# Performance work log

Measured on AMD Instinct MI355X. Metric: run time of the kernel, lower is better.

## Reference

```python
import jax, jax.numpy as jnp
import numpy as np
from jax import lax

B_, DIM, H, W, Dd = 2, 256, 16, 16, 16
DI, N, DTR, K = 256, 8, 16, 4   # d_inner (expand=1), d_state, dt_rank=ceil(256/16), d_conv
OUT_C = 1200
L = H * W * Dd
EPS = 1e-5


def setup_inputs() -> dict:
    key = jax.random.key(0)
    ks = jax.random.split(key, 20)
    g = lambda k, s: jax.random.normal(k, s, jnp.float32) * 0.02
    A_log = jnp.log(jnp.broadcast_to(jnp.arange(1, N + 1, dtype=jnp.float32), (DI, N)))
    dt_bias = jnp.full((DI,), float(np.log(np.expm1(0.01))), jnp.float32)
    return {
        "input0": jax.random.normal(ks[0], (B_, DIM, H, W, Dd), jnp.float32),
        "input1": jax.random.normal(ks[1], (B_, DIM, H, W, Dd), jnp.float32),
        "norm0_w": jnp.ones((DIM,), jnp.float32),
        "norm0_b": jnp.zeros((DIM,), jnp.float32),
        "norm1_w": jnp.ones((DIM,), jnp.float32),
        "norm1_b": jnp.zeros((DIM,), jnp.float32),
        "in_proj_w": g(ks[2], (DI, DIM)),
        "in_projz_w": g(ks[3], (DI, DIM)),
        "conv1d_w": g(ks[4], (DI, 1, K)),
        "conv1d_bias": jnp.zeros((DI,), jnp.float32),
        "conv1db_w": g(ks[5], (DI, 1, K)),
        "conv1db_bias": jnp.zeros((DI,), jnp.float32),
        "xproj_w": g(ks[6], (DTR + 2 * N, DI)),
        "xprojb_w": g(ks[7], (DTR + 2 * N, DI)),
        "dtproj_w": g(ks[8], (DI, DTR)),
        "dtproj_bias": dt_bias,
        "dtprojb_w": g(ks[9], (DI, DTR)),
        "dtprojb_bias": dt_bias,
        "A_log": A_log,
        "Ab_log": A_log,
        "D_p": jnp.ones((DI,), jnp.float32),
        "D_b": jnp.ones((DI,), jnp.float32),
        "rms_w": jnp.ones((DI,), jnp.float32),
        "out_proj_w": g(ks[10], (DIM, DI)),
        "conv3d_w": g(ks[11], (OUT_C, DIM)),
        "conv3d_bias": jnp.zeros((OUT_C,), jnp.float32),
    }


def _layernorm(x, w, b):
    m = x.mean(-1, keepdims=True)
    v = ((x - m) ** 2).mean(-1, keepdims=True)
    return (x - m) * lax.rsqrt(v + EPS) * w + b


def _rmsnorm(x, w):
    return x * lax.rsqrt((x * x).mean(-1, keepdims=True) + EPS) * w


def _ssm_dir(x, z, conv_w, conv_b, xproj_w, dtproj_w, dtproj_bias, A_log, Dp):
    # One direction of the bimamba-v2 selective scan. x, z: (b, L, d_inner)
    xt = x.transpose(0, 2, 1)  # (b, d, L)
    xc = lax.conv_general_dilated(xt, conv_w, (1,), [(K - 1, 0)], feature_group_count=DI)
    x = jax.nn.silu(xc + conv_b[None, :, None]).transpose(0, 2, 1)  # causal dw-conv + silu
    dbl = x @ xproj_w.T                                   # (b, L, dt_rank + 2n)
    dt, Bm, Cm = dbl[..., :DTR], dbl[..., DTR:DTR + N], dbl[..., DTR + N:]
    dt = jax.nn.softplus(dt @ dtproj_w.T + dtproj_bias)    # (b, L, d)
    A = -jnp.exp(A_log)                                    # (d, n)
    dA = jnp.exp(dt[..., None] * A)                        # (b, L, d, n)
    dBu = (dt * x)[..., None] * Bm[:, :, None, :]          # (b, L, d, n)

    def step(h, inp):
        dA_t, dBu_t, C_t = inp
        h = h * dA_t + dBu_t
        return h, jnp.einsum('bdn,bn->bd', h, C_t)

    h0 = jnp.zeros((x.shape[0], DI, N), x.dtype)
    _, ys = lax.scan(step, h0, (dA.transpose(1, 0, 2, 3), dBu.transpose(1, 0, 2, 3), Cm.transpose(1, 0, 2)))
    y = ys.transpose(1, 0, 2) + x * Dp                     # (b, L, d)
    return y * jax.nn.silu(z)                              # gate from the matching branch


def _forward(input0, input1, norm0_w, norm0_b, norm1_w, norm1_b, in_proj_w, in_projz_w,
             conv1d_w, conv1d_bias, conv1db_w, conv1db_bias, xproj_w, xprojb_w,
             dtproj_w, dtproj_bias, dtprojb_w, dtprojb_bias, A_log, Ab_log,
             D_p, D_b, rms_w, out_proj_w, conv3d_w, conv3d_bias):
    b = input0.shape[0]
    skip = input0
    seq0 = input0.transpose(0, 2, 3, 4, 1).reshape(b, L, DIM)  # b (h w d) c
    seq1 = input1.transpose(0, 2, 3, 4, 1).reshape(b, L, DIM)
    seq0 = _layernorm(seq0, norm0_w, norm0_b)
    seq1 = _layernorm(seq1, norm1_w, norm1_b)
    x = seq0 @ in_proj_w.T    # SSM input from input0
    z = seq1 @ in_projz_w.T   # gate from extra_emb (input1)
    y_f = _ssm_dir(x, z, conv1d_w, conv1d_bias, xproj_w, dtproj_w, dtproj_bias, A_log, D_p)
    y_b = _ssm_dir(x[:, ::-1], z[:, ::-1], conv1db_w, conv1db_bias, xprojb_w,
                   dtprojb_w, dtprojb_bias, Ab_log, D_b)[:, ::-1]

    def head(y):
        o = _rmsnorm(y, rms_w) @ out_proj_w.T              # use_norm=True, then out_proj
        o = o.reshape(b, H, W, Dd, DIM).transpose(0, 4, 1, 2, 3) + skip
        return jnp.einsum('bchwd,oc->bohwd', o, conv3d_w) + conv3d_bias[None, :, None, None, None]

    out = head((y_f + y_b) * 0.5)   # if_devide_out=True
    return out, head(y_f), head(y_b)


def reference(input0, input1, norm0_w, norm0_b, norm1_w, norm1_b, in_proj_w, in_projz_w,
              conv1d_w, conv1d_bias, conv1db_w, conv1db_bias, xproj_w, xprojb_w,
              dtproj_w, dtproj_bias, dtprojb_w, dtprojb_bias, A_log, Ab_log,
              D_p, D_b, rms_w, out_proj_w, conv3d_w, conv3d_bias):
    return _forward(input0, input1, norm0_w, norm0_b, norm1_w, norm1_b, in_proj_w, in_projz_w,
                    conv1d_w, conv1d_bias, conv1db_w, conv1db_bias, xproj_w, xprojb_w,
                    dtproj_w, dtproj_bias, dtprojb_w, dtprojb_bias, A_log, Ab_log,
                    D_p, D_b, rms_w, out_proj_w, conv3d_w, conv3d_bias)
```

## Files before the change

kernel.cpp:

```cpp
#include <hip/hip_runtime.h>
#include <cstdint>

#define NTOK 8192

typedef __attribute__((ext_vector_type(4))) float f32x4;
typedef __attribute__((ext_vector_type(8))) short s16x8;
typedef __attribute__((ext_vector_type(4))) short s16x4;

__device__ __forceinline__ short f2bf(float f) {
  union { float f; unsigned u; } x; x.f = f;
  unsigned r = x.u + 0x7FFFu + ((x.u >> 16) & 1u);
  return (short)(r >> 16);
}
__device__ __forceinline__ float bf2f(short s) {
  union { float f; unsigned u; } x;
  x.u = ((unsigned)(unsigned short)s) << 16;
  return x.f;
}
__device__ __forceinline__ void gl_lds16(const void* g, void* l) {
  __builtin_amdgcn_global_load_lds((const unsigned int*)g, (unsigned int*)l, 16, 0, 0);
}

__global__ __launch_bounds__(256) void ln_transpose_kernel(
    const float* __restrict__ in0, const float* __restrict__ in1,
    const float* __restrict__ w0, const float* __restrict__ b0,
    const float* __restrict__ w1, const float* __restrict__ b1,
    const float* __restrict__ wxp, const float* __restrict__ wzp,
    const float* __restrict__ wop, const float* __restrict__ wcp,
    short* __restrict__ Wx, short* __restrict__ Wz,
    short* __restrict__ Wo, short* __restrict__ Wc,
    short* __restrict__ xlnz)
{
  __shared__ float tile[32 * 257];
  __shared__ float mu[32], rs[32];
  const int tid  = threadIdx.x;
  const int pass = blockIdx.x >> 8;
  const int b    = (blockIdx.x >> 7) & 1;
  const int l0   = (blockIdx.x & 127) << 5;

  {
    int base = (int)blockIdx.x << 10;
    #pragma unroll
    for (int i = 0; i < 4; ++i) {
      int idx = base + (i << 8) + tid;
      if (idx < 65536)       Wx[idx] = f2bf(wxp[idx]);
      else if (idx < 131072) Wz[idx - 65536] = f2bf(wzp[idx - 65536]);
      else if (idx < 196608) Wo[idx - 131072] = f2bf(wop[idx - 131072]);
      else {
        int k = idx - 196608;
        Wc[k] = ((k >> 8) < 1200) ? f2bf(wcp[k]) : (short)0;
      }
    }
  }

  const float* in = pass ? in1 : in0;
  #pragma unroll 8
  for (int i = 0; i < 32; ++i) {
    int e = (i << 8) + tid;
    int c = e >> 5, lo = e & 31;
    tile[lo * 257 + c] = in[((size_t)(b * 256 + c) << 12) + l0 + lo];
  }
  __syncthreads();
  if (tid < 64) {
    int r = tid & 31, hh = tid >> 5;
    float s = 0.f, ss = 0.f;
    #pragma unroll 16
    for (int c = hh * 128; c < hh * 128 + 128; ++c) {
      float v = tile[r * 257 + c];
      s += v; ss += v * v;
    }
    s  += __shfl_xor(s, 32, 64);
    ss += __shfl_xor(ss, 32, 64);
    if (hh == 0) {
      float m = s * (1.f / 256.f);
      mu[r] = m;
      rs[r] = rsqrtf(ss * (1.f / 256.f) - m * m + 1e-5f);
    }
  }
  __syncthreads();
  const float* w  = pass ? w1 : w0;
  const float* bb = pass ? b1 : b0;
  float wv = w[tid], bv = bb[tid];
  #pragma unroll 8
  for (int i = 0; i < 32; ++i) {
    float v = tile[i * 257 + tid];
    int row = (pass ? 8192 : 0) + (b << 12) + l0 + i;
    xlnz[(size_t)row * 256 + tid] = f2bf((v - mu[i]) * rs[i] * wv + bv);
  }
}

template <int EPI>
__global__ __launch_bounds__(256) void gemm_fast(
    const short* __restrict__ A, const short* __restrict__ W0,
    const short* __restrict__ W1, float* __restrict__ Cf,
    short* __restrict__ Cb, const float* __restrict__ ADD,
    const float* __restrict__ bias, int Msplit)
{
  __shared__ short As[2][4096];
  __shared__ short Bs[2][4096];
  const int tid  = threadIdx.x;
  const int lane = tid & 63, wave = tid >> 6;
  const int m0 = blockIdx.y << 7;
  const int n0 = blockIdx.x << 7;
  const short* W = (EPI == 0 && m0 >= Msplit) ? W1 : W0;

  const int sr = tid >> 2;
  const int sc = (tid & 3) << 3;
  const int mf = lane & 15, kq = lane >> 4;
  const int wm = (wave & 1) << 6, wn = (wave >> 1) << 6;

  const short* Ar0 = A + (size_t)(m0 + sr) * 256 + sc;
  const short* Ar1 = A + (size_t)(m0 + 64 + sr) * 256 + sc;
  const short* Br0 = W + (size_t)(n0 + sr) * 256 + sc;
  const short* Br1 = W + (size_t)(n0 + 64 + sr) * 256 + sc;
  const int wo = wave << 9;

  f32x4 acc[4][4] = {};

  gl_lds16(Ar0, &As[0][wo]);
  gl_lds16(Ar1, &As[0][wo + 2048]);
  gl_lds16(Br0, &Bs[0][wo]);
  gl_lds16(Br1, &Bs[0][wo + 2048]);
  __syncthreads();

  #pragma unroll
  for (int t = 0; t < 8; ++t) {
    const int cur = t & 1;
    if (t < 7) {
      const int kt = (t + 1) << 5;
      gl_lds16(Ar0 + kt, &As[cur ^ 1][wo]);
      gl_lds16(Ar1 + kt, &As[cur ^ 1][wo + 2048]);
      gl_lds16(Br0 + kt, &Bs[cur ^ 1][wo]);
      gl_lds16(Br1 + kt, &Bs[cur ^ 1][wo + 2048]);
    }
    s16x8 af[4], bfr[4];
    #pragma unroll
    for (int i = 0; i < 4; ++i)
      af[i] = *(const s16x8*)&As[cur][((wm + (i << 4) + mf) << 5) + (kq << 3)];
    #pragma unroll
    for (int j = 0; j < 4; ++j)
      bfr[j] = *(const s16x8*)&Bs[cur][((wn + (j << 4) + mf) << 5) + (kq << 3)];
    #pragma unroll
    for (int i = 0; i < 4; ++i)
      #pragma unroll
      for (int j = 0; j < 4; ++j)
        acc[i][j] = __builtin_amdgcn_mfma_f32_16x16x32_bf16(af[i], bfr[j], acc[i][j], 0, 0, 0);
    __syncthreads();
  }

  if (EPI == 0) {
    #pragma unroll
    for (int i = 0; i < 4; ++i) {
      int gm = m0 + wm + (i << 4) + (kq << 2);
      #pragma unroll
      for (int j = 0; j < 4; ++j) {
        int gn = n0 + wn + (j << 4) + mf;
        #pragma unroll
        for (int r = 0; r < 4; ++r)
          Cf[(size_t)(gm + r) * 256 + gn] = acc[i][j][r];
      }
    }
  } else {
    const int head = m0 >> 13, bb = (m0 >> 12) & 1, lb = m0 & 4095;
    float* obase = Cf + (size_t)head * (2u * 1200u * 4096u) + (size_t)bb * (1200u * 4096u);
    #pragma unroll
    for (int i = 0; i < 4; ++i) {
      int l = lb + wm + (i << 4) + (kq << 2);
      #pragma unroll
      for (int j = 0; j < 4; ++j) {
        int gn = n0 + wn + (j << 4) + mf;
        if (gn < 1200) {
          float bv = bias[gn];
          f32x4 v = acc[i][j];
          v[0] += bv; v[1] += bv; v[2] += bv; v[3] += bv;
          __builtin_nontemporal_store(v, (f32x4*)&obase[(size_t)gn * 4096 + l]);
        }
      }
    }
  }
}

__global__ __launch_bounds__(256) void fused_front(
    const float* __restrict__ x,
    const float* __restrict__ cw0, const float* __restrict__ cb0,
    const float* __restrict__ cw1, const float* __restrict__ cb1,
    const float* __restrict__ xw0, const float* __restrict__ xw1,
    const float* __restrict__ dtw0, const float* __restrict__ dtb0,
    const float* __restrict__ dtw1, const float* __restrict__ dtb1,
    const float* __restrict__ Alog0, const float* __restrict__ Alog1,
    float* __restrict__ xcg, float* __restrict__ dblg,
    float* __restrict__ P, float* __restrict__ Q)
{
  __shared__ float xcs[16 * 256];
  __shared__ short wxs[256 * 33];
  __shared__ float dls[512];
  const int tid = threadIdx.x;
  const int dir = blockIdx.x >> 9;
  const int b   = (blockIdx.x >> 8) & 1;
  const int ch  = blockIdx.x & 255;
  const int t0  = ch << 4;
  const float* cw   = dir ? cw1 : cw0;
  const float* cb   = dir ? cb1 : cb0;
  const float* xw   = dir ? xw1 : xw0;
  const float* dtw  = dir ? dtw1 : dtw0;
  const float* dtb  = dir ? dtb1 : dtb0;
  const float* Alog = dir ? Alog1 : Alog0;
  const size_t dS = (size_t)dir * (NTOK * 256);
  const size_t xb = ((size_t)b) << 12;

  {
    const int d = tid;
    const float w0 = cw[(d << 2)], w1 = cw[(d << 2) + 1],
                w2 = cw[(d << 2) + 2], w3 = cw[(d << 2) + 3];
    const float bias = cb[d];
    float h0 = 0.f, h1 = 0.f, h2 = 0.f;
    #pragma unroll
    for (int i = 0; i < 3; ++i) {
      int ts = t0 - 3 + i; float v = 0.f;
      if (ts >= 0) { int tn = dir ? 4095 - ts : ts; v = x[(xb + tn) * 256 + d]; }
      h0 = h1; h1 = h2; h2 = v;
    }
    #pragma unroll
    for (int s = 0; s < 16; ++s) {
      int ts = t0 + s;
      int tn = dir ? 4095 - ts : ts;
      float xv = x[(xb + tn) * 256 + d];
      float a = bias + w0 * h0 + w1 * h1 + w2 * h2 + w3 * xv;
      h0 = h1; h1 = h2; h2 = xv;
      float v = a / (1.f + __expf(-a));
      xcs[s * 256 + d] = v;
      xcg[dS + (xb + ts) * 256 + d] = v;
    }
  }
  #pragma unroll
  for (int i = 0; i < 32; ++i) {
    int flat = (i << 8) + tid;
    wxs[(flat & 255) * 33 + (flat >> 8)] = f2bf(xw[flat]);
  }
  __syncthreads();

  {
    const int j = tid & 31, s0 = tid >> 5;
    float a0 = 0.f, a1 = 0.f;
    #pragma unroll 8
    for (int r = 0; r < 256; ++r) {
      float w = bf2f(wxs[r * 33 + j]);
      a0 = fmaf(xcs[s0 * 256 + r], w, a0);
      a1 = fmaf(xcs[(s0 + 8) * 256 + r], w, a1);
    }
    dls[(s0 << 5) + j] = a0;
    dls[((s0 + 8) << 5) + j] = a1;
    size_t db = (size_t)dir * 262144 + ((xb + t0) << 5);
    dblg[db + tid] = a0;
    dblg[db + 256 + tid] = a1;
  }
  __syncthreads();

  {
    const int d = tid;
    float wrow[16];
    #pragma unroll
    for (int r = 0; r < 16; ++r) wrow[r] = dtw[(d << 4) + r];
    const float bias = dtb[d];
    float Av[8], p[8], q[8];
    #pragma unroll
    for (int n = 0; n < 8; ++n) {
      Av[n] = -expf(Alog[(d << 3) + n]); p[n] = 1.f; q[n] = 0.f;
    }
    for (int s = 0; s < 16; ++s) {
      float a = bias;
      #pragma unroll
      for (int r = 0; r < 16; ++r) a = fmaf(dls[(s << 5) + r], wrow[r], a);
      float dtv = (a > 20.f) ? a : log1pf(__expf(a));
      float xv = xcs[s * 256 + d];
      float du = dtv * xv;
      #pragma unroll
      for (int n = 0; n < 8; ++n) {
        float dA = __expf(dtv * Av[n]);
        p[n] *= dA;
        q[n] = fmaf(q[n], dA, du * dls[(s << 5) + 16 + n]);
      }
    }
    size_t ob = (size_t)dir * 1048576 + ((size_t)((b << 8) + ch) * 8) * 256 + d;
    #pragma unroll
    for (int n = 0; n < 8; ++n) { P[ob + (n << 8)] = p[n]; Q[ob + (n << 8)] = q[n]; }
  }
}

__global__ __launch_bounds__(64) void scan_p2(
    const float* __restrict__ P, const float* __restrict__ Q, float* __restrict__ Hs)
{
  const int d   = ((blockIdx.x & 3) << 6) + threadIdx.x;
  const int bid = blockIdx.x >> 2;
  const int dir = bid >> 4, b = (bid >> 3) & 1, n = bid & 7;
  const size_t dOff = (size_t)dir * 1048576;
  float h = 0.f;
  #pragma unroll 8
  for (int ch = 0; ch < 256; ++ch) {
    size_t i = dOff + ((size_t)((b << 8) + ch) * 8 + n) * 256 + d;
    Hs[i] = h;
    h = fmaf(P[i], h, Q[i]);
  }
}

__global__ __launch_bounds__(256) void scan_p3(
    const float* __restrict__ xcg, const float* __restrict__ dblg,
    const float* __restrict__ dtw0, const float* __restrict__ dtb0,
    const float* __restrict__ dtw1, const float* __restrict__ dtb1,
    const float* __restrict__ Hs, const float* __restrict__ z,
    const float* __restrict__ Alog0, const float* __restrict__ Alog1,
    const float* __restrict__ Dp0, const float* __restrict__ Dp1,
    short* __restrict__ yall)
{
  __shared__ float dl[512];
  const int d = threadIdx.x;
  const int dir = blockIdx.x >> 9;
  const int b   = (blockIdx.x >> 8) & 1;
  const int ch  = blockIdx.x & 255;
  const int t0  = ch << 4;
  const float* dtw  = dir ? dtw1 : dtw0;
  const float* dtb  = dir ? dtb1 : dtb0;
  const float* Alog = dir ? Alog1 : Alog0;
  const float* Dp   = dir ? Dp1 : Dp0;
  const size_t dS = (size_t)dir * (NTOK * 256);
  const size_t xb = ((size_t)b) << 12;
  short* y = yall + (size_t)dir * (NTOK * 256);

  size_t db = (size_t)dir * 262144 + ((xb + t0) << 5);
  dl[d]       = dblg[db + d];
  dl[256 + d] = dblg[db + 256 + d];
  float wrow[16];
  #pragma unroll
  for (int r = 0; r < 16; ++r) wrow[r] = dtw[(d << 4) + r];
  const float bias = dtb[d];
  float Av[8], h[8];
  #pragma unroll
  for (int n = 0; n < 8; ++n) Av[n] = -expf(Alog[(d << 3) + n]);
  size_t hb = (size_t)dir * 1048576 + ((size_t)((b << 8) + ch) * 8) * 256 + d;
  #pragma unroll
  for (int n = 0; n < 8; ++n) h[n] = Hs[hb + (n << 8)];
  const float Dv = Dp[d];
  __syncthreads();
  for (int s = 0; s < 16; ++s) {
    float a = bias;
    #pragma unroll
    for (int r = 0; r < 16; ++r) a = fmaf(dl[(s << 5) + r], wrow[r], a);
    float dtv = (a > 20.f) ? a : log1pf(__expf(a));
    int ts = t0 + s;
    float xv = xcg[dS + (xb + ts) * 256 + d];
    float du = dtv * xv;
    float yv = 0.f;
    #pragma unroll
    for (int n = 0; n < 8; ++n) {
      float dA = __expf(dtv * Av[n]);
      h[n] = fmaf(h[n], dA, du * dl[(s << 5) + 16 + n]);
      yv = fmaf(h[n], dl[(s << 5) + 24 + n], yv);
    }
    yv = fmaf(xv, Dv, yv);
    int tn = dir ? (4095 - ts) : ts;
    size_t zi = (xb + tn) * 256 + d;
    float zv = z[zi];
    y[zi] = f2bf(yv * zv / (1.f + __expf(-zv)));
  }
}

__global__ __launch_bounds__(256) void gemm_rms_epi1(
    const short* __restrict__ yall, const short* __restrict__ W0,
    const float* __restrict__ rmsw, short* __restrict__ Cb,
    const float* __restrict__ in0)
{
  __shared__ short As[4096];
  __shared__ short Bs[4096];
  __shared__ float scale[128];
  __shared__ float rw[256];
  const int tid  = threadIdx.x;
  const int lane = tid & 63, wave = tid >> 6;
  const int m0 = blockIdx.y << 7;
  const int n0 = blockIdx.x << 7;
  const int mode = m0 >> 13;
  const int tok0 = m0 & 8191;
  const short* yf = yall;
  const short* yb = yall + 2097152;
  const short* ysel = (mode == 1) ? yf : yb;

  rw[tid] = rmsw[tid];

  for (int rr = 0; rr < 32; ++rr) {
    int r = (rr << 2) + wave;
    size_t base = (size_t)(tok0 + r) * 256 + (lane << 2);
    float v0, v1, v2, v3;
    if (mode == 0) {
      s16x4 a = *(const s16x4*)&yf[base];
      s16x4 c = *(const s16x4*)&yb[base];
      v0 = 0.5f * (bf2f(a[0]) + bf2f(c[0]));
      v1 = 0.5f * (bf2f(a[1]) + bf2f(c[1]));
      v2 = 0.5f * (bf2f(a[2]) + bf2f(c[2]));
      v3 = 0.5f * (bf2f(a[3]) + bf2f(c[3]));
    } else {
      s16x4 a = *(const s16x4*)&ysel[base];
      v0 = bf2f(a[0]); v1 = bf2f(a[1]); v2 = bf2f(a[2]); v3 = bf2f(a[3]);
    }
    float ss = v0 * v0 + v1 * v1 + v2 * v2 + v3 * v3;
    #pragma unroll
    for (int o = 32; o > 0; o >>= 1) ss += __shfl_xor(ss, o, 64);
    if (lane == 0) scale[r] = rsqrtf(ss * (1.f / 256.f) + 1e-5f);
  }
  __syncthreads();

  const int sr = tid >> 2;
  const int sc = (tid & 3) << 3;
  const int mf = lane & 15, kq = lane >> 4;
  const int wm = (wave & 1) << 6, wn = (wave >> 1) << 6;
  const short* Br0 = W0 + (size_t)(n0 + sr) * 256 + sc;
  const short* Br1 = W0 + (size_t)(n0 + 64 + sr) * 256 + sc;
  const int wo = wave << 9;

  const int ar = tid >> 1;
  const int ac = (tid & 1) << 4;
  const size_t abase = (size_t)(tok0 + ar) * 256 + ac;
  const float s_r = scale[ar];

  f32x4 acc[4][4] = {};

  for (int t = 0; t < 8; ++t) {
    const int kt = t << 5;
    {
      s16x8 o0, o1;
      if (mode == 0) {
        s16x8 f0 = *(const s16x8*)&yf[abase + kt];
        s16x8 f1 = *(const s16x8*)&yf[abase + kt + 8];
        s16x8 c0 = *(const s16x8*)&yb[abase + kt];
        s16x8 c1 = *(const s16x8*)&yb[abase + kt + 8];
        #pragma unroll
        for (int e = 0; e < 8; ++e) {
          o0[e] = f2bf((0.5f * (bf2f(f0[e]) + bf2f(c0[e])) * s_r) * rw[kt + ac + e]);
          o1[e] = f2bf((0.5f * (bf2f(f1[e]) + bf2f(c1[e])) * s_r) * rw[kt + ac + 8 + e]);
        }
      } else {
        s16x8 f0 = *(const s16x8*)&ysel[abase + kt];
        s16x8 f1 = *(const s16x8*)&ysel[abase + kt + 8];
        #pragma unroll
        for (int e = 0; e < 8; ++e) {
          o0[e] = f2bf((bf2f(f0[e]) * s_r) * rw[kt + ac + e]);
          o1[e] = f2bf((bf2f(f1[e]) * s_r) * rw[kt + ac + 8 + e]);
        }
      }
      *(s16x8*)&As[(ar << 5) + ac]     = o0;
      *(s16x8*)&As[(ar << 5) + ac + 8] = o1;
    }
    gl_lds16(Br0 + kt, &Bs[wo]);
    gl_lds16(Br1 + kt, &Bs[wo + 2048]);
    __syncthreads();
    s16x8 af[4], bfr[4];
    #pragma unroll
    for (int i = 0; i < 4; ++i)
      af[i] = *(const s16x8*)&As[((wm + (i << 4) + mf) << 5) + (kq << 3)];
    #pragma unroll
    for (int j = 0; j < 4; ++j)
      bfr[j] = *(const s16x8*)&Bs[((wn + (j << 4) + mf) << 5) + (kq << 3)];
    #pragma unroll
    for (int i = 0; i < 4; ++i)
      #pragma unroll
      for (int j = 0; j < 4; ++j)
        acc[i][j] = __builtin_amdgcn_mfma_f32_16x16x32_bf16(af[i], bfr[j], acc[i][j], 0, 0, 0);
    __syncthreads();
  }

  #pragma unroll
  for (int i = 0; i < 4; ++i) {
    int gm = m0 + wm + (i << 4) + (kq << 2);
    int tok = gm & 8191;
    int bb2 = tok >> 12, ll = tok & 4095;
    #pragma unroll
    for (int j = 0; j < 4; ++j) {
      int gn = n0 + wn + (j << 4) + mf;
      f32x4 sk = *(const f32x4*)&in0[((((size_t)(bb2 << 8)) + gn) << 12) + ll];
      #pragma unroll
      for (int r = 0; r < 4; ++r) {
        float v = acc[i][j][r] + sk[r];
        Cb[(size_t)(gm + r) * 256 + gn] = f2bf(v);
      }
    }
  }
}

extern "C" void kernel_launch(void* const* d_in, const int* in_sizes, int n_in,
                              void* d_out, int out_size, void* d_ws, size_t ws_size,
                              hipStream_t stream) {
  const float* in0        = (const float*)d_in[0];
  const float* in1        = (const float*)d_in[1];
  const float* n0w        = (const float*)d_in[2];
  const float* n0b        = (const float*)d_in[3];
  const float* n1w        = (const float*)d_in[4];
  const float* n1b        = (const float*)d_in[5];
  const float* in_proj_w  = (const float*)d_in[6];
  const float* in_projz_w = (const float*)d_in[7];
  const float* conv1d_w   = (const float*)d_in[8];
  const float* conv1d_b   = (const float*)d_in[9];
  const float* conv1db_w  = (const float*)d_in[10];
  const float* conv1db_b  = (const float*)d_in[11];
  const float* xproj_w    = (const float*)d_in[12];
  const float* xprojb_w   = (const float*)d_in[13];
  const float* dtproj_w   = (const float*)d_in[14];
  const float* dtproj_b   = (const float*)d_in[15];
  const float* dtprojb_w  = (const float*)d_in[16];
  const float* dtprojb_b  = (const float*)d_in[17];
  const float* A_log      = (const float*)d_in[18];
  const float* Ab_log     = (const float*)d_in[19];
  const float* D_p        = (const float*)d_in[20];
  const float* D_b        = (const float*)d_in[21];
  const float* rms_w      = (const float*)d_in[22];
  const float* out_proj_w = (const float*)d_in[23];
  const float* conv3d_w   = (const float*)d_in[24];
  const float* conv3d_b   = (const float*)d_in[25];
  (void)in_sizes; (void)n_in; (void)out_size; (void)ws_size;

  float* ws = (float*)d_ws;
  size_t o = 0;
  short* xlnz = (short*)(ws + o); o += 2097152;
  float* x    = ws + o;           o += 2097152;
  float* z    = ws + o;           o += 2097152;
  float* xc2  = ws + o;           o += 4194304;
  float* dbl2 = ws + o;           o += 524288;
  float* P    = ws + o;           o += 2097152;
  float* Q    = ws + o;           o += 2097152;
  float* Hs   = ws + o;           o += 2097152;
  short* yall = (short*)(ws + o); o += 2097152;
  short* obuf = (short*)(ws + o); o += 3145728;
  short* Wx   = (short*)(ws + o); o += 32768;
  short* Wz   = (short*)(ws + o); o += 32768;
  short* Wo   = (short*)(ws + o); o += 32768;
  short* Wc   = (short*)(ws + o); o += 163840;
  float* out  = (float*)d_out;

  dim3 blk(256);

  ln_transpose_kernel<<<dim3(512), blk, 0, stream>>>(
      in0, in1, n0w, n0b, n1w, n1b,
      in_proj_w, in_projz_w, out_proj_w, conv3d_w, Wx, Wz, Wo, Wc,
      xlnz);

  gemm_fast<0><<<dim3(2, 128), blk, 0, stream>>>(xlnz, Wx, Wz, x, nullptr, nullptr, nullptr, 8192);

  fused_front<<<dim3(1024), blk, 0, stream>>>(
      x, conv1d_w, conv1d_b, conv1db_w, conv1db_b,
      xproj_w, xprojb_w, dtproj_w, dtproj_b, dtprojb_w, dtprojb_b,
      A_log, Ab_log, xc2, dbl2, P, Q);

  scan_p2<<<dim3(128), dim3(64), 0, stream>>>(P, Q, Hs);

  scan_p3<<<dim3(1024), blk, 0, stream>>>(
      xc2, dbl2, dtproj_w, dtproj_b, dtprojb_w, dtprojb_b,
      Hs, z, A_log, Ab_log, D_p, D_b, yall);

  gemm_rms_epi1<<<dim3(2, 192), blk, 0, stream>>>(yall, Wo, rms_w, obuf, in0);
  gemm_fast<2><<<dim3(10, 192), blk, 0, stream>>>(obuf, Wc, nullptr, out, nullptr, nullptr, conv3d_b, 0);
}
```

Before: 345.5 us.

## Vectorize LDS reads in scan kernels and halve M tile of RMS out-proj GEMM

```diff
diff --git a/kernel.cpp b/kernel.cpp
--- a/kernel.cpp
+++ b/kernel.cpp
@@ -192,7 +192,7 @@
     float* __restrict__ P, float* __restrict__ Q)
 {
   __shared__ float xcs[16 * 256];
-  __shared__ short wxs[256 * 33];
+  __shared__ short wxs[32 * 264];
   __shared__ float dls[512];
   const int tid = threadIdx.x;
   const int dir = blockIdx.x >> 9;
@@ -233,20 +233,35 @@
     }
   }
   #pragma unroll
-  for (int i = 0; i < 32; ++i) {
-    int flat = (i << 8) + tid;
-    wxs[(flat & 255) * 33 + (flat >> 8)] = f2bf(xw[flat]);
-  }
+  for (int i = 0; i < 32; ++i)
+    wxs[i * 264 + tid] = f2bf(xw[(i << 8) + tid]);
   __syncthreads();
 
   {
     const int j = tid & 31, s0 = tid >> 5;
     float a0 = 0.f, a1 = 0.f;
-    #pragma unroll 8
-    for (int r = 0; r < 256; ++r) {
-      float w = bf2f(wxs[r * 33 + j]);
-      a0 = fmaf(xcs[s0 * 256 + r], w, a0);
-      a1 = fmaf(xcs[(s0 + 8) * 256 + r], w, a1);
+    const short* wr = &wxs[j * 264];
+    const float* xa = &xcs[s0 * 256];
+    const float* xbp = &xcs[(s0 + 8) * 256];
+    #pragma unroll 4
+    for (int rb = 0; rb < 32; ++rb) {
+      s16x8 w8 = *(const s16x8*)&wr[rb << 3];
+      f32x4 p0 = *(const f32x4*)&xa[rb << 3];
+      f32x4 p1 = *(const f32x4*)&xa[(rb << 3) + 4];
+      f32x4 q0 = *(const f32x4*)&xbp[rb << 3];
+      f32x4 q1 = *(const f32x4*)&xbp[(rb << 3) + 4];
+      #pragma unroll
+      for (int e = 0; e < 4; ++e) {
+        float w = bf2f(w8[e]);
+        a0 = fmaf(p0[e], w, a0);
+        a1 = fmaf(q0[e], w, a1);
+      }
+      #pragma unroll
+      for (int e = 0; e < 4; ++e) {
+        float w = bf2f(w8[4 + e]);
+        a0 = fmaf(p1[e], w, a0);
+        a1 = fmaf(q1[e], w, a1);
+      }
     }
     dls[(s0 << 5) + j] = a0;
     dls[((s0 + 8) << 5) + j] = a1;
@@ -268,17 +283,31 @@
       Av[n] = -expf(Alog[(d << 3) + n]); p[n] = 1.f; q[n] = 0.f;
     }
     for (int s = 0; s < 16; ++s) {
+      const float* dlp = &dls[s << 5];
+      f32x4 d0 = *(const f32x4*)&dlp[0];
+      f32x4 d1 = *(const f32x4*)&dlp[4];
+      f32x4 d2 = *(const f32x4*)&dlp[8];
+      f32x4 d3 = *(const f32x4*)&dlp[12];
       float a = bias;
       #pragma unroll
-      for (int r = 0; r < 16; ++r) a = fmaf(dls[(s << 5) + r], wrow[r], a);
+      for (int e = 0; e < 4; ++e) a = fmaf(d0[e], wrow[e], a);
+      #pragma unroll
+      for (int e = 0; e < 4; ++e) a = fmaf(d1[e], wrow[4 + e], a);
+      #pragma unroll
+      for (int e = 0; e < 4; ++e) a = fmaf(d2[e], wrow[8 + e], a);
+      #pragma unroll
+      for (int e = 0; e < 4; ++e) a = fmaf(d3[e], wrow[12 + e], a);
       float dtv = (a > 20.f) ? a : log1pf(__expf(a));
       float xv = xcs[s * 256 + d];
       float du = dtv * xv;
+      float Bv[8];
+      *(f32x4*)&Bv[0] = *(const f32x4*)&dlp[16];
+      *(f32x4*)&Bv[4] = *(const f32x4*)&dlp[20];
       #pragma unroll
       for (int n = 0; n < 8; ++n) {
         float dA = __expf(dtv * Av[n]);
         p[n] *= dA;
-        q[n] = fmaf(q[n], dA, du * dls[(s << 5) + 16 + n]);
+        q[n] = fmaf(q[n], dA, du * Bv[n]);
       }
     }
     size_t ob = (size_t)dir * 1048576 + ((size_t)((b << 8) + ch) * 8) * 256 + d;
@@ -342,19 +371,35 @@
   const float Dv = Dp[d];
   __syncthreads();
   for (int s = 0; s < 16; ++s) {
+    const float* dlp = &dl[s << 5];
+    f32x4 d0 = *(const f32x4*)&dlp[0];
+    f32x4 d1 = *(const f32x4*)&dlp[4];
+    f32x4 d2 = *(const f32x4*)&dlp[8];
+    f32x4 d3 = *(const f32x4*)&dlp[12];
     float a = bias;
     #pragma unroll
-    for (int r = 0; r < 16; ++r) a = fmaf(dl[(s << 5) + r], wrow[r], a);
+    for (int e = 0; e < 4; ++e) a = fmaf(d0[e], wrow[e], a);
+    #pragma unroll
+    for (int e = 0; e < 4; ++e) a = fmaf(d1[e], wrow[4 + e], a);
+    #pragma unroll
+    for (int e = 0; e < 4; ++e) a = fmaf(d2[e], wrow[8 + e], a);
+    #pragma unroll
+    for (int e = 0; e < 4; ++e) a = fmaf(d3[e], wrow[12 + e], a);
     float dtv = (a > 20.f) ? a : log1pf(__expf(a));
     int ts = t0 + s;
     float xv = xcg[dS + (xb + ts) * 256 + d];
     float du = dtv * xv;
+    float Bv[8], Cv[8];
+    *(f32x4*)&Bv[0] = *(const f32x4*)&dlp[16];
+    *(f32x4*)&Bv[4] = *(const f32x4*)&dlp[20];
+    *(f32x4*)&Cv[0] = *(const f32x4*)&dlp[24];
+    *(f32x4*)&Cv[4] = *(const f32x4*)&dlp[28];
     float yv = 0.f;
     #pragma unroll
     for (int n = 0; n < 8; ++n) {
       float dA = __expf(dtv * Av[n]);
-      h[n] = fmaf(h[n], dA, du * dl[(s << 5) + 16 + n]);
-      yv = fmaf(h[n], dl[(s << 5) + 24 + n], yv);
+      h[n] = fmaf(h[n], dA, du * Bv[n]);
+      yv = fmaf(h[n], Cv[n], yv);
     }
     yv = fmaf(xv, Dv, yv);
     int tn = dir ? (4095 - ts) : ts;
@@ -369,13 +414,13 @@
     const float* __restrict__ rmsw, short* __restrict__ Cb,
     const float* __restrict__ in0)
 {
-  __shared__ short As[4096];
+  __shared__ short As[2048];
   __shared__ short Bs[4096];
-  __shared__ float scale[128];
+  __shared__ float scale[64];
   __shared__ float rw[256];
   const int tid  = threadIdx.x;
   const int lane = tid & 63, wave = tid >> 6;
-  const int m0 = blockIdx.y << 7;
+  const int m0 = blockIdx.y << 6;
   const int n0 = blockIdx.x << 7;
   const int mode = m0 >> 13;
   const int tok0 = m0 & 8191;
@@ -385,7 +430,7 @@
 
   rw[tid] = rmsw[tid];
 
-  for (int rr = 0; rr < 32; ++rr) {
+  for (int rr = 0; rr < 16; ++rr) {
     int r = (rr << 2) + wave;
     size_t base = (size_t)(tok0 + r) * 256 + (lane << 2);
     float v0, v1, v2, v3;
@@ -410,69 +455,61 @@
   const int sr = tid >> 2;
   const int sc = (tid & 3) << 3;
   const int mf = lane & 15, kq = lane >> 4;
-  const int wm = (wave & 1) << 6, wn = (wave >> 1) << 6;
+  const int wn = wave << 5;
   const short* Br0 = W0 + (size_t)(n0 + sr) * 256 + sc;
   const short* Br1 = W0 + (size_t)(n0 + 64 + sr) * 256 + sc;
   const int wo = wave << 9;
 
-  const int ar = tid >> 1;
-  const int ac = (tid & 1) << 4;
+  const int ar = tid >> 2;
+  const int ac = (tid & 3) << 3;
   const size_t abase = (size_t)(tok0 + ar) * 256 + ac;
   const float s_r = scale[ar];
 
-  f32x4 acc[4][4] = {};
+  f32x4 acc[4][2] = {};
 
   for (int t = 0; t < 8; ++t) {
     const int kt = t << 5;
     {
-      s16x8 o0, o1;
+      s16x8 o0;
       if (mode == 0) {
         s16x8 f0 = *(const s16x8*)&yf[abase + kt];
-        s16x8 f1 = *(const s16x8*)&yf[abase + kt + 8];
         s16x8 c0 = *(const s16x8*)&yb[abase + kt];
-        s16x8 c1 = *(const s16x8*)&yb[abase + kt + 8];
         #pragma unroll
-        for (int e = 0; e < 8; ++e) {
+        for (int e = 0; e < 8; ++e)
           o0[e] = f2bf((0.5f * (bf2f(f0[e]) + bf2f(c0[e])) * s_r) * rw[kt + ac + e]);
-          o1[e] = f2bf((0.5f * (bf2f(f1[e]) + bf2f(c1[e])) * s_r) * rw[kt + ac + 8 + e]);
-        }
       } else {
         s16x8 f0 = *(const s16x8*)&ysel[abase + kt];
-        s16x8 f1 = *(const s16x8*)&ysel[abase + kt + 8];
         #pragma unroll
-        for (int e = 0; e < 8; ++e) {
+        for (int e = 0; e < 8; ++e)
           o0[e] = f2bf((bf2f(f0[e]) * s_r) * rw[kt + ac + e]);
-          o1[e] = f2bf((bf2f(f1[e]) * s_r) * rw[kt + ac + 8 + e]);
-        }
-      }
-      *(s16x8*)&As[(ar << 5) + ac]     = o0;
-      *(s16x8*)&As[(ar << 5) + ac + 8] = o1;
+      }
+      *(s16x8*)&As[(ar << 5) + ac] = o0;
     }
     gl_lds16(Br0 + kt, &Bs[wo]);
     gl_lds16(Br1 + kt, &Bs[wo + 2048]);
     __syncthreads();
-    s16x8 af[4], bfr[4];
+    s16x8 af[4], bfr[2];
     #pragma unroll
     for (int i = 0; i < 4; ++i)
-      af[i] = *(const s16x8*)&As[((wm + (i << 4) + mf) << 5) + (kq << 3)];
-    #pragma unroll
-    for (int j = 0; j < 4; ++j)
+      af[i] = *(const s16x8*)&As[(((i << 4) + mf) << 5) + (kq << 3)];
+    #pragma unroll
+    for (int j = 0; j < 2; ++j)
       bfr[j] = *(const s16x8*)&Bs[((wn + (j << 4) + mf) << 5) + (kq << 3)];
     #pragma unroll
     for (int i = 0; i < 4; ++i)
       #pragma unroll
-      for (int j = 0; j < 4; ++j)
+      for (int j = 0; j < 2; ++j)
         acc[i][j] = __builtin_amdgcn_mfma_f32_16x16x32_bf16(af[i], bfr[j], acc[i][j], 0, 0, 0);
     __syncthreads();
   }
 
   #pragma unroll
   for (int i = 0; i < 4; ++i) {
-    int gm = m0 + wm + (i << 4) + (kq << 2);
+    int gm = m0 + (i << 4) + (kq << 2);
     int tok = gm & 8191;
     int bb2 = tok >> 12, ll = tok & 4095;
     #pragma unroll
-    for (int j = 0; j < 4; ++j) {
+    for (int j = 0; j < 2; ++j) {
       int gn = n0 + wn + (j << 4) + mf;
       f32x4 sk = *(const f32x4*)&in0[((((size_t)(bb2 << 8)) + gn) << 12) + ll];
       #pragma unroll
@@ -553,6 +590,6 @@
       xc2, dbl2, dtproj_w, dtproj_b, dtprojb_w, dtprojb_b,
       Hs, z, A_log, Ab_log, D_p, D_b, yall);
 
-  gemm_rms_epi1<<<dim3(2, 192), blk, 0, stream>>>(yall, Wo, rms_w, obuf, in0);
+  gemm_rms_epi1<<<dim3(2, 384), blk, 0, stream>>>(yall, Wo, rms_w, obuf, in0);
   gemm_fast<2><<<dim3(10, 192), blk, 0, stream>>>(obuf, Wc, nullptr, out, nullptr, nullptr, conv3d_b, 0);
 }
```

New measurement: 333.5 us (median of 2 runs). 1.04x faster.
